# Optimization experiments

Measured on AMD Instinct MI355X. Metric: run time of the kernel, lower is better.

Reference implementation:

```python
import jax, jax.numpy as jnp
import numpy as np

B = 512; S = 6; Q = 2            # meta-batch, n_way*k_shot, n_way*q_query
DIM = 64; IMG = 28; N_WAY = 2
HEADS = 4; HD = DIM // HEADS     # retrieval heads / head dim
EPS = 1e-5


def _pool_mat(inp, out):
    # exact torch AdaptiveAvgPool2d windowing as a matrix [out, inp]
    P = np.zeros((out, inp), np.float32)
    for i in range(out):
        s = (i * inp) // out
        e = -((-(i + 1) * inp) // out)
        P[i, s:e] = 1.0 / (e - s)
    return jnp.asarray(P)

P28 = _pool_mat(IMG, 8)  # 28 -> 8; subsequent 8 -> 8 pools are identity


def _gelu(x):
    return jax.nn.gelu(x, approximate=False)


def _conv(x, w, b):
    y = jax.lax.conv_general_dilated(x, w, (1, 1), ((1, 1), (1, 1)),
                                     dimension_numbers=('NCHW', 'OIHW', 'NCHW'))
    return y + b[None, :, None, None]


def _bn(x, p):
    # p rows: gamma, beta, running_mean, running_var (eval-mode BatchNorm2d)
    g, bt, m, v = p[0], p[1], p[2], p[3]
    sc = g / jnp.sqrt(v + EPS)
    return (x - m[None, :, None, None]) * sc[None, :, None, None] + bt[None, :, None, None]


def _img_in(x, c1w, c1b, bn1, c2w, c2b, bn2, c3w, c3b, bn3, c4w, c4b, bn4, lin_w):
    h = _bn(_conv(x, c1w, c1b), bn1)
    h = jnp.einsum('oi,ncij,pj->ncop', P28, h, P28)   # adaptive avg pool 28x28 -> 8x8
    h = _gelu(h)                                       # dropout is identity in eval
    h = _gelu(_bn(_conv(h, c2w, c2b), bn2))
    h = _gelu(_bn(_conv(h, c3w, c3b), bn3))
    h = _gelu(_bn(_conv(h, c4w, c4b), bn4))            # -> [N,1,8,8]
    h = h.reshape(h.shape[0], -1)                      # [N,64]
    return h @ lin_w.T                                 # Linear(64 -> DIM, no bias)


def _net(x, w1, w2):
    # x: [B,K,D]; w1,w2: [B,D,D] batched fast weights
    h = jnp.einsum('bed,bkd->bke', w1, x)
    ah = _gelu(h)
    y = jnp.einsum('bed,bkd->bke', w2, ah)
    return y, h


def _get_lor(x, w1, w2, r_q, r_k, r_v, r_o, ln_w, ln_b):
    b, k, _ = x.shape
    q, _ = _net(x, w1, w2)
    qh = jnp.einsum('nhd,bkd->bknh', r_q, q)
    sc = jnp.einsum('bknh,rnh->bknr', qh, r_k) / (HD ** 0.5)
    p = jax.nn.softmax(sc, axis=-1)
    lor = jnp.einsum('bknr,rnh->bknh', p, r_v).reshape(b, k, DIM)
    lor = jnp.einsum('de,bkd->bke', r_o, lor)
    z = lor + x
    mu = z.mean(-1, keepdims=True)
    var = ((z - mu) ** 2).mean(-1, keepdims=True)
    return (z - mu) / jnp.sqrt(var + EPS) * ln_w + ln_b


def _forward(query_w, sxs, qxs, inner_lr, c1w, c1b, bn1, c2w, c2b, bn2, c3w, c3b, bn3,
             c4w, c4b, bn4, lin_w, emb, w1, w2, tags, r_q, r_k, r_v, r_o, ln_w, ln_b,
             sys, qys):
    b = query_w.shape[0]
    s = sxs.shape[1]
    q = qxs.shape[1]
    feats = lambda im: _img_in(im.reshape(-1, 1, IMG, IMG), c1w, c1b, bn1, c2w, c2b,
                               bn2, c3w, c3b, bn3, c4w, c4b, bn4, lin_w)
    sx = feats(sxs).reshape(b, s, DIM)
    qx = feats(qxs).reshape(b, q, DIM)
    qe = tags[4]
    w1b = jnp.broadcast_to(w1, (b, DIM, DIM))
    w2b = jnp.broadcast_to(w2, (b, DIM, DIM))
    bound = sx + emb[sys]                                          # [B,S,D]
    # all 4 tag variants for all S shots in one vectorized get_lor call
    inp = (bound[:, :, None, :] + tags[:4][None, None]).reshape(b, s * 4, DIM)
    lors = _get_lor(inp, w1b, w2b, r_q, r_k, r_v, r_o, ln_w, ln_b).reshape(b, s, 4, DIM)
    l1s, r1s, l2s, r2s = lors[:, :, 0], lors[:, :, 1], lors[:, :, 2], lors[:, :, 3]
    qw1 = w1[None] + jnp.einsum('bsl,bsr->blr', l1s, r1s)
    qw2 = w2[None] + jnp.einsum('bsl,bsr->blr', l2s, r2s)
    preds, _ = _net(qx + qe, qw1, qw2)                             # [B,Q,D]
    logits = jnp.einsum('ld,bqd->bql', emb, preds).reshape(-1, N_WAY)
    labels = qys.reshape(-1)
    ls = jax.nn.log_softmax(logits)
    task_loss = -jnp.take_along_axis(ls, labels[:, None], axis=1).mean()
    n_correct = (jnp.argmax(logits, axis=1) == labels).sum()
    return task_loss, n_correct, b * q


def setup_inputs() -> dict:
    key = jax.random.key(0)
    ks = jax.random.split(key, 24)
    rn = lambda i, sh, sc=1.0: sc * jax.random.normal(ks[i], sh, jnp.float32)
    def bnp(i, c):
        k0, k1, k2 = jax.random.split(ks[i], 3)
        return jnp.stack([1.0 + 0.1 * jax.random.normal(k0, (c,)),
                          0.1 * jax.random.normal(k1, (c,)),
                          0.1 * jax.random.normal(k2, (c,)),
                          0.5 + jax.random.uniform(jax.random.fold_in(ks[i], 3), (c,))])
    return {
        'query_w': rn(0, (B, DIM)),
        'sxs': rn(1, (B, S, IMG * IMG)),
        'qxs': rn(2, (B, Q, IMG * IMG)),
        'inner_lr': jnp.float32(0.1),
        'c1w': rn(3, (32, 1, 3, 3), 0.3), 'c1b': rn(4, (32,), 0.1), 'bn1': bnp(5, 32),
        'c2w': rn(6, (32, 32, 3, 3), 0.06), 'c2b': rn(7, (32,), 0.1), 'bn2': bnp(8, 32),
        'c3w': rn(9, (32, 32, 3, 3), 0.06), 'c3b': rn(10, (32,), 0.1), 'bn3': bnp(11, 32),
        'c4w': rn(12, (1, 32, 3, 3), 0.06), 'c4b': rn(13, (1,), 0.1), 'bn4': bnp(14, 1),
        'lin_w': rn(15, (DIM, 64), 0.125),
        'emb': rn(16, (N_WAY, DIM), 0.125),
        'w1': rn(17, (DIM, DIM), 0.125),
        'w2': rn(18, (DIM, DIM), 0.125),
        'tags': rn(19, (8, DIM), 0.125),
        'r_q': rn(20, (HEADS, HD, DIM), 0.125),
        'r_k': rn(21, (16, HEADS, HD), 0.25),
        'r_v': rn(22, (16, HEADS, HD), 0.25),
        'r_o': rn(23, (DIM, DIM), 0.125),
        'ln_w': 0.001 * jnp.ones((DIM,), jnp.float32),
        'ln_b': jnp.zeros((DIM,), jnp.float32),
        'sys': jax.random.randint(jax.random.fold_in(key, 100), (B, S), 0, N_WAY),
        'qys': jax.random.randint(jax.random.fold_in(key, 101), (B, Q), 0, N_WAY),
    }


def reference(query_w, sxs, qxs, inner_lr, c1w, c1b, bn1, c2w, c2b, bn2, c3w, c3b, bn3,
              c4w, c4b, bn4, lin_w, emb, w1, w2, tags, r_q, r_k, r_v, r_o, ln_w, ln_b,
              sys, qys):
    task_loss, n_correct, n_q = _forward(query_w, sxs, qxs, inner_lr, c1w, c1b, bn1,
                                         c2w, c2b, bn2, c3w, c3b, bn3, c4w, c4b, bn4,
                                         lin_w, emb, w1, w2, tags, r_q, r_k, r_v, r_o,
                                         ln_w, ln_b, sys, qys)
    return (task_loss, task_loss, jnp.float32(0.0), n_correct, n_q)
```

## Files before the change

kernel.cpp:

```cpp
#include <hip/hip_runtime.h>
#include <math.h>

constexpr int NSUP = 3072;
constexpr float EPSF = 1e-5f;

constexpr int WS_W1B  = 0;
constexpr int WS_B1   = 1024;
constexpr int WS_W2B  = 1056;
constexpr int WS_W3B  = 5664;
constexpr int WS_W4B  = 10272;
constexpr int WS_B4   = 10416;
constexpr int WS_B2   = 10420;
constexpr int WS_B3   = 10452;
constexpr int WS_HW1  = 10484;
constexpr int WS_HW2  = 12788;
constexpr int WS_HRQ  = 15092;
constexpr int WS_HROT = 17396;
constexpr int WS_PART = 19700;
constexpr int WS_FEATS= 20724;

using short8 = __attribute__((ext_vector_type(8))) short;
using f32x4  = __attribute__((ext_vector_type(4))) float;

__device__ __forceinline__ float gelu_f(float x) {
    return 0.5f * x * (1.0f + erff(x * 0.70710678118654752440f));
}
__device__ __forceinline__ unsigned short f2bf(float f) {
    unsigned u = __float_as_uint(f);
    return (unsigned short)((u + 0x7FFFu + ((u >> 16) & 1u)) >> 16);
}
__device__ __forceinline__ float bflo(unsigned u) { return __uint_as_float(u << 16); }
__device__ __forceinline__ float bfhi(unsigned u) { return __uint_as_float(u & 0xffff0000u); }

__global__ void __launch_bounds__(256) precompute_kernel(
    const float* __restrict__ c1w, const float* __restrict__ c1b, const float* __restrict__ bn1,
    const float* __restrict__ c2w, const float* __restrict__ c2b, const float* __restrict__ bn2,
    const float* __restrict__ c3w, const float* __restrict__ c3b, const float* __restrict__ bn3,
    const float* __restrict__ c4w, const float* __restrict__ c4b, const float* __restrict__ bn4,
    const float* __restrict__ w1, const float* __restrict__ w2,
    const float* __restrict__ rq, const float* __restrict__ ro,
    float* __restrict__ ws)
{
    const int gid = blockIdx.x * 256 + threadIdx.x;
    const int gsz = gridDim.x * 256;

    unsigned short* w1b = (unsigned short*)(ws + WS_W1B);
    for (int v = gid; v < 2048; v += gsz) {
        int kt = v >> 10, rem = v & 1023, oc = rem >> 5, kk = rem & 31;
        int tap = kt * 32 + kk;
        unsigned short o = 0;
        if (tap < 36) {
            int tt = tap / 6, s = tap - tt * 6;
            float sum = 0.f;
            for (int di = 0; di < 3; ++di) {
                int a = tt - di; if (a < 0 || a > 3) continue;
                for (int dj = 0; dj < 3; ++dj) {
                    int bb = s - dj; if (bb < 0 || bb > 3) continue;
                    sum += c1w[oc * 9 + di * 3 + dj];
                }
            }
            float sc1 = bn1[oc] * rsqrtf(bn1[96 + oc] + EPSF);
            o = f2bf(sum * sc1 * (1.0f / 16.0f));
        }
        w1b[v] = o;
    }
    for (int c = gid; c < 32; c += gsz) {
        float sc1 = bn1[c] * rsqrtf(bn1[96 + c] + EPSF);
        ws[WS_B1 + c] = (c1b[c] - bn1[64 + c]) * sc1 + bn1[32 + c];
        float sc2 = bn2[c] * rsqrtf(bn2[96 + c] + EPSF);
        ws[WS_B2 + c] = (c2b[c] - bn2[64 + c]) * sc2 + bn2[32 + c];
        float sc3 = bn3[c] * rsqrtf(bn3[96 + c] + EPSF);
        ws[WS_B3 + c] = (c3b[c] - bn3[64 + c]) * sc3 + bn3[32 + c];
    }
    unsigned short* w2b = (unsigned short*)(ws + WS_W2B);
    unsigned short* w3b = (unsigned short*)(ws + WS_W3B);
    for (int v = gid; v < 9216; v += gsz) {
        int tap = v >> 10, oc = (v >> 5) & 31, ic = v & 31;
        float sc2 = bn2[oc] * rsqrtf(bn2[96 + oc] + EPSF);
        float sc3 = bn3[oc] * rsqrtf(bn3[96 + oc] + EPSF);
        w2b[v] = f2bf(c2w[oc * 288 + ic * 9 + tap] * sc2);
        w3b[v] = f2bf(c3w[oc * 288 + ic * 9 + tap] * sc3);
    }
    {
        unsigned short* w4b = (unsigned short*)(ws + WS_W4B);
        float sc4 = bn4[0] * rsqrtf(bn4[3] + EPSF);
        for (int v = gid; v < 288; v += gsz) {
            int tap = v >> 5, ic = v & 31;
            w4b[v] = f2bf(c4w[ic * 9 + tap] * sc4);
        }
        if (gid == 0) ws[WS_B4] = (c4b[0] - bn4[2]) * sc4 + bn4[1];
    }
    unsigned short* hw1 = (unsigned short*)(ws + WS_HW1);
    unsigned short* hw2 = (unsigned short*)(ws + WS_HW2);
    unsigned short* hrq = (unsigned short*)(ws + WS_HRQ);
    unsigned short* hro = (unsigned short*)(ws + WS_HROT);
    for (int v = gid; v < 4608; v += gsz) {
        int e = v / 72, d = v - e * 72;
        unsigned short a = 0, b = 0, c = 0, r = 0;
        if (d < 64) {
            a = f2bf(w1[e * 64 + d]);
            b = f2bf(w2[e * 64 + d]);
            c = f2bf(rq[e * 64 + d]);
            r = f2bf(ro[d * 64 + e]);
        }
        hw1[v] = a; hw2[v] = b; hrq[v] = c; hro[v] = r;
    }
}

__global__ void __launch_bounds__(512, 4) feats_kernel(
    const float* __restrict__ sxs, const float* __restrict__ qxs,
    const float* __restrict__ lin_w, const float* __restrict__ ws,
    float* __restrict__ feats)
{
    __shared__ __align__(16) unsigned short sAct[8][3200];
    __shared__ __align__(16) unsigned short sWB[9216];
    __shared__ __align__(16) float sh4[8][64];

    const int t    = threadIdx.x;
    const int wv   = t >> 6;
    const int lane = t & 63;
    const int col  = lane & 15;
    const int quad = lane >> 4;
    const int n    = blockIdx.x * 8 + wv;

    unsigned short* A = sAct[wv];

    {
        uint4 z = {0, 0, 0, 0};
        for (int i = t; i < 3200; i += 512) ((uint4*)sAct)[i] = z;
        if (t < 256) ((uint4*)sWB)[t] = ((const uint4*)(ws + WS_W1B))[t];
    }
    __syncthreads();

    {
        const float* img = (n < NSUP) ? (sxs + (size_t)n * 784) : (qxs + (size_t)(n - NSUP) * 784);
        int ttj[8], ssj[8];
        #pragma unroll
        for (int j = 0; j < 8; ++j) {
            int k = quad * 8 + j;
            ttj[j] = k / 6; ssj[j] = k - ttj[j] * 6;
        }
        f32x4 acc[4][2];
        #pragma unroll
        for (int mt = 0; mt < 4; ++mt) { acc[mt][0] = (f32x4){0,0,0,0}; acc[mt][1] = (f32x4){0,0,0,0}; }

        short8 b00 = *(const short8*)(sWB + (0 * 32 + 0 * 16 + col) * 32 + quad * 8);
        short8 b01 = *(const short8*)(sWB + (0 * 32 + 1 * 16 + col) * 32 + quad * 8);
        short8 b10 = *(const short8*)(sWB + (1 * 32 + 0 * 16 + col) * 32 + quad * 8);
        short8 b11 = *(const short8*)(sWB + (1 * 32 + 1 * 16 + col) * 32 + quad * 8);

        #pragma unroll
        for (int mt = 0; mt < 4; ++mt) {
            int px = mt * 16 + col;
            int sr = (((px >> 3) * 7) >> 1) - 1;
            int sc = (((px & 7) * 7) >> 1) - 1;
            short8 a0;
            #pragma unroll
            for (int j = 0; j < 8; ++j) {
                int rr = sr + ttj[j], cc = sc + ssj[j];
                float v = ((unsigned)rr < 28u && (unsigned)cc < 28u) ? img[rr * 28 + cc] : 0.f;
                a0[j] = (short)f2bf(v);
            }
            acc[mt][0] = __builtin_amdgcn_mfma_f32_16x16x32_bf16(a0, b00, acc[mt][0], 0, 0, 0);
            acc[mt][1] = __builtin_amdgcn_mfma_f32_16x16x32_bf16(a0, b01, acc[mt][1], 0, 0, 0);
            short8 a1 = {0,0,0,0,0,0,0,0};
            if (quad == 0) {
                #pragma unroll
                for (int j = 0; j < 4; ++j) {
                    int rr = sr + 5, cc = sc + 2 + j;
                    float v = ((unsigned)rr < 28u && (unsigned)cc < 28u) ? img[rr * 28 + cc] : 0.f;
                    a1[j] = (short)f2bf(v);
                }
            }
            acc[mt][0] = __builtin_amdgcn_mfma_f32_16x16x32_bf16(a1, b10, acc[mt][0], 0, 0, 0);
            acc[mt][1] = __builtin_amdgcn_mfma_f32_16x16x32_bf16(a1, b11, acc[mt][1], 0, 0, 0);
        }
        float bi0 = ws[WS_B1 + col], bi1 = ws[WS_B1 + 16 + col];
        #pragma unroll
        for (int mt = 0; mt < 4; ++mt)
            #pragma unroll
            for (int reg = 0; reg < 4; ++reg) {
                int px = mt * 16 + quad * 4 + reg;
                unsigned short* dst = A + (((px >> 3) + 1) * 10 + (px & 7) + 1) * 32;
                dst[col]      = f2bf(gelu_f(acc[mt][0][reg] + bi0));
                dst[col + 16] = f2bf(gelu_f(acc[mt][1][reg] + bi1));
            }
    }
    __syncthreads();
    for (int i = t; i < 1152; i += 512) ((uint4*)sWB)[i] = ((const uint4*)(ws + WS_W2B))[i];
    __syncthreads();

    #pragma unroll 1
    for (int layer = 0; layer < 2; ++layer) {
        f32x4 acc[4][2];
        #pragma unroll
        for (int mt = 0; mt < 4; ++mt) { acc[mt][0] = (f32x4){0,0,0,0}; acc[mt][1] = (f32x4){0,0,0,0}; }
        const unsigned short* abase[4];
        #pragma unroll
        for (int mt = 0; mt < 4; ++mt) {
            int px = mt * 16 + col;
            abase[mt] = A + ((px >> 3) * 10 + (px & 7)) * 32 + quad * 8;
        }
        #pragma unroll
        for (int dr = 0; dr < 3; ++dr)
            #pragma unroll
            for (int dc = 0; dc < 3; ++dc) {
                int tap = dr * 3 + dc;
                short8 b0 = *(const short8*)(sWB + (tap * 32 + col) * 32 + quad * 8);
                short8 b1 = *(const short8*)(sWB + (tap * 32 + 16 + col) * 32 + quad * 8);
                #pragma unroll
                for (int mt = 0; mt < 4; ++mt) {
                    short8 a = *(const short8*)(abase[mt] + (dr * 10 + dc) * 32);
                    acc[mt][0] = __builtin_amdgcn_mfma_f32_16x16x32_bf16(a, b0, acc[mt][0], 0, 0, 0);
                    acc[mt][1] = __builtin_amdgcn_mfma_f32_16x16x32_bf16(a, b1, acc[mt][1], 0, 0, 0);
                }
            }
        float bi0 = ws[(layer ? WS_B3 : WS_B2) + col];
        float bi1 = ws[(layer ? WS_B3 : WS_B2) + 16 + col];
        #pragma unroll
        for (int mt = 0; mt < 4; ++mt)
            #pragma unroll
            for (int reg = 0; reg < 4; ++reg) {
                int px = mt * 16 + quad * 4 + reg;
                unsigned short* dst = A + (((px >> 3) + 1) * 10 + (px & 7) + 1) * 32;
                dst[col]      = f2bf(gelu_f(acc[mt][0][reg] + bi0));
                dst[col + 16] = f2bf(gelu_f(acc[mt][1][reg] + bi1));
            }
        __syncthreads();
        if (layer == 0) {
            for (int i = t; i < 1152; i += 512) ((uint4*)sWB)[i] = ((const uint4*)(ws + WS_W3B))[i];
            __syncthreads();
        }
    }

    {
        f32x4 acc4[4];
        #pragma unroll
        for (int mt = 0; mt < 4; ++mt) acc4[mt] = (f32x4){0,0,0,0};
        const unsigned short* abase[4];
        #pragma unroll
        for (int mt = 0; mt < 4; ++mt) {
            int px = mt * 16 + col;
            abase[mt] = A + ((px >> 3) * 10 + (px & 7)) * 32 + quad * 8;
        }
        const unsigned short* w4g = (const unsigned short*)(ws + WS_W4B);
        #pragma unroll
        for (int dr = 0; dr < 3; ++dr)
            #pragma unroll
            for (int dc = 0; dc < 3; ++dc) {
                int tap = dr * 3 + dc;
                short8 b = *(const short8*)(w4g + tap * 32 + quad * 8);
                #pragma unroll
                for (int mt = 0; mt < 4; ++mt) {
                    short8 a = *(const short8*)(abase[mt] + (dr * 10 + dc) * 32);
                    acc4[mt] = __builtin_amdgcn_mfma_f32_16x16x32_bf16(a, b, acc4[mt], 0, 0, 0);
                }
            }
        if (col < 4) {
            f32x4 v = acc4[0];
            if (col == 1) v = acc4[1];
            else if (col == 2) v = acc4[2];
            else if (col == 3) v = acc4[3];
            float b4 = ws[WS_B4];
            #pragma unroll
            for (int reg = 0; reg < 4; ++reg)
                sh4[wv][col * 16 + quad * 4 + reg] = gelu_f(v[reg] + b4);
        }
    }
    __syncthreads();

    {
        const float4* lw = (const float4*)(lin_w + (size_t)lane * 64);
        const float4* hp = (const float4*)sh4[wv];
        float acc = 0.f;
        #pragma unroll
        for (int j = 0; j < 16; ++j) {
            float4 w = lw[j], h = hp[j];
            acc += w.x * h.x + w.y * h.y + w.z * h.z + w.w * h.w;
        }
        feats[n * 64 + lane] = acc;
    }
}

__device__ __forceinline__ void head_gemm(const unsigned short* __restrict__ Ab,
                                          const unsigned short* __restrict__ Bw,
                                          int col, int quad, int wvid, f32x4 res[2])
{
    #pragma unroll
    for (int u = 0; u < 2; ++u) {
        int tau = wvid + u * 4;
        int mt = tau & 1, nt = tau >> 1;
        f32x4 acc = {0, 0, 0, 0};
        #pragma unroll
        for (int kt = 0; kt < 2; ++kt) {
            short8 a = *(const short8*)(Ab + (mt * 16 + col) * 72 + kt * 32 + quad * 8);
            short8 b = *(const short8*)(Bw + (nt * 16 + col) * 72 + kt * 32 + quad * 8);
            acc = __builtin_amdgcn_mfma_f32_16x16x32_bf16(a, b, acc, 0, 0, 0);
        }
        res[u] = acc;
    }
}

__global__ void __launch_bounds__(256, 2) head_kernel(
    const float* __restrict__ emb, const float* __restrict__ tags,
    const float* __restrict__ rk, const float* __restrict__ rv,
    const float* __restrict__ lnw, const float* __restrict__ lnb,
    const int* __restrict__ sys, const int* __restrict__ qys,
    const float* __restrict__ ws, const float* __restrict__ feats,
    float* __restrict__ part)
{
    __shared__ __align__(16) unsigned short sW1B[4608], sW2B[4608], sRQB[4608], sROT[4608];
    __shared__ __align__(16) unsigned short bufA[2304], bufB[2304];
    __shared__ __align__(16) float sXf[1536];
    __shared__ __align__(16) float s_xq[128], s_ah[128], s_yp[128];
    __shared__ float s_t1[12], s_t2[12], s_mu[24], s_rs[24], s_lg[4];

    const int t    = threadIdx.x;
    const int b    = blockIdx.x;
    const int wvid = t >> 6;
    const int col  = t & 15;
    const int quad = (t >> 4) & 3;

    for (int i = t; i < 576; i += 256) {
        ((uint4*)sW1B)[i] = ((const uint4*)(ws + WS_HW1))[i];
        ((uint4*)sW2B)[i] = ((const uint4*)(ws + WS_HW2))[i];
        ((uint4*)sRQB)[i] = ((const uint4*)(ws + WS_HRQ))[i];
        ((uint4*)sROT)[i] = ((const uint4*)(ws + WS_HROT))[i];
    }
    if (t < 72) {
        uint4 z = {0, 0, 0, 0};
        ((uint4*)(bufA + 1728))[t] = z;
        ((uint4*)(bufB + 1728))[t] = z;
    }
    for (int idx = t; idx < 1536; idx += 256) {
        int k = idx >> 6, e = idx & 63;
        int s = k >> 2, tg = k & 3;
        int cls = sys[b * 6 + s];
        float v = feats[(b * 6 + s) * 64 + e] + emb[cls * 64 + e] + tags[tg * 64 + e];
        sXf[idx] = v;
        bufA[k * 72 + e] = f2bf(v);
    }
    __syncthreads();

    f32x4 r[2];
    head_gemm(bufA, sW1B, col, quad, wvid, r);
    #pragma unroll
    for (int u = 0; u < 2; ++u) {
        int tau = wvid + u * 4, mt = tau & 1, nt = tau >> 1;
        #pragma unroll
        for (int reg = 0; reg < 4; ++reg) {
            int row = mt * 16 + quad * 4 + reg;
            if (row < 24) bufB[row * 72 + nt * 16 + col] = f2bf(gelu_f(r[u][reg]));
        }
    }
    __syncthreads();
    head_gemm(bufB, sW2B, col, quad, wvid, r);
    #pragma unroll
    for (int u = 0; u < 2; ++u) {
        int tau = wvid + u * 4, mt = tau & 1, nt = tau >> 1;
        #pragma unroll
        for (int reg = 0; reg < 4; ++reg) {
            int row = mt * 16 + quad * 4 + reg;
            if (row < 24) bufA[row * 72 + nt * 16 + col] = f2bf(r[u][reg]);
        }
    }
    __syncthreads();
    head_gemm(bufA, sRQB, col, quad, wvid, r);
    #pragma unroll
    for (int u = 0; u < 2; ++u) {
        int tau = wvid + u * 4, mt = tau & 1, nt = tau >> 1;
        #pragma unroll
        for (int reg = 0; reg < 4; ++reg) {
            int row = mt * 16 + quad * 4 + reg;
            if (row < 24) bufB[row * 72 + nt * 16 + col] = f2bf(r[u][reg]);
        }
    }
    __syncthreads();

    if (t < 96) {
        int k = t >> 2, nn = t & 3;
        const unsigned short* qp = bufB + k * 72 + nn * 16;
        uint4 u0 = *(const uint4*)(qp);
        uint4 u1 = *(const uint4*)(qp + 8);
        float qv[16];
        qv[0]=bflo(u0.x); qv[1]=bfhi(u0.x); qv[2]=bflo(u0.y); qv[3]=bfhi(u0.y);
        qv[4]=bflo(u0.z); qv[5]=bfhi(u0.z); qv[6]=bflo(u0.w); qv[7]=bfhi(u0.w);
        qv[8]=bflo(u1.x); qv[9]=bfhi(u1.x); qv[10]=bflo(u1.y); qv[11]=bfhi(u1.y);
        qv[12]=bflo(u1.z); qv[13]=bfhi(u1.z); qv[14]=bflo(u1.w); qv[15]=bfhi(u1.w);
        float sc[16]; float mx = -1e30f;
        #pragma unroll
        for (int rr = 0; rr < 16; ++rr) {
            const float* kp = rk + rr * 64 + nn * 16;
            float d = 0.f;
            #pragma unroll
            for (int h = 0; h < 16; ++h) d += qv[h] * kp[h];
            d *= 0.25f;
            sc[rr] = d; mx = fmaxf(mx, d);
        }
        float sum = 0.f;
        #pragma unroll
        for (int rr = 0; rr < 16; ++rr) { sc[rr] = expf(sc[rr] - mx); sum += sc[rr]; }
        float inv = 1.0f / sum;
        float o[16];
        #pragma unroll
        for (int h = 0; h < 16; ++h) o[h] = 0.f;
        #pragma unroll
        for (int rr = 0; rr < 16; ++rr) {
            const float* vp = rv + rr * 64 + nn * 16;
            float p = sc[rr];
            #pragma unroll
            for (int h = 0; h < 16; ++h) o[h] += p * vp[h];
        }
        unsigned short* op = bufA + k * 72 + nn * 16;
        #pragma unroll
        for (int h = 0; h < 16; ++h) op[h] = f2bf(o[h] * inv);
    }
    __syncthreads();

    head_gemm(bufA, sROT, col, quad, wvid, r);
    #pragma unroll
    for (int u = 0; u < 2; ++u) {
        int tau = wvid + u * 4, mt = tau & 1, nt = tau >> 1;
        #pragma unroll
        for (int reg = 0; reg < 4; ++reg) {
            int row = mt * 16 + quad * 4 + reg;
            if (row < 24) {
                int idx = row * 64 + nt * 16 + col;
                sXf[idx] = sXf[idx] + r[u][reg];
            }
        }
    }
    __syncthreads();

    if (t < 24) {
        const float4* zp = (const float4*)(sXf + t * 64);
        float sx_ = 0.f;
        #pragma unroll
        for (int j = 0; j < 16; ++j) {
            float4 v = zp[(j + t) & 15];
            sx_ += v.x + v.y + v.z + v.w;
        }
        float mu = sx_ * (1.0f / 64.0f);
        float vv = 0.f;
        #pragma unroll
        for (int j = 0; j < 16; ++j) {
            float4 v = zp[(j + t) & 15];
            float d0 = v.x - mu, d1 = v.y - mu, d2 = v.z - mu, d3 = v.w - mu;
            vv += d0*d0 + d1*d1 + d2*d2 + d3*d3;
        }
        s_mu[t] = mu;
        s_rs[t] = 1.0f / sqrtf(vv * (1.0f / 64.0f) + EPSF);
    }
    __syncthreads();
    for (int idx = t; idx < 1536; idx += 256) {
        int k = idx >> 6, e = idx & 63;
        float v = (sXf[idx] - s_mu[k]) * s_rs[k] * lnw[e] + lnb[e];
        bufB[k * 72 + e] = f2bf(v);
    }
    if (t < 128) {
        int q = t >> 6, e = t & 63;
        s_xq[t] = feats[(NSUP + b * 2 + q) * 64 + e] + tags[256 + e];
    }
    __syncthreads();

    if (t < 12) {
        int q = t / 6, s = t - q * 6;
        const uint4* rp = (const uint4*)(bufB + (s * 4 + 1) * 72);
        const float* xp = s_xq + q * 64;
        float d = 0.f;
        #pragma unroll
        for (int j = 0; j < 8; ++j) {
            uint4 u = rp[j];
            const float* x = xp + j * 8;
            d += bflo(u.x)*x[0] + bfhi(u.x)*x[1] + bflo(u.y)*x[2] + bfhi(u.y)*x[3]
               + bflo(u.z)*x[4] + bfhi(u.z)*x[5] + bflo(u.w)*x[6] + bfhi(u.w)*x[7];
        }
        s_t1[t] = d;
    }
    __syncthreads();
    if (t < 128) {
        int q = t >> 6, e = t & 63;
        const uint4* wp = (const uint4*)(sW1B + e * 72);
        const float* xp = s_xq + q * 64;
        float acc = 0.f;
        #pragma unroll
        for (int j = 0; j < 8; ++j) {
            uint4 u = wp[j];
            const float* x = xp + j * 8;
            acc += bflo(u.x)*x[0] + bfhi(u.x)*x[1] + bflo(u.y)*x[2] + bfhi(u.y)*x[3]
                 + bflo(u.z)*x[4] + bfhi(u.z)*x[5] + bflo(u.w)*x[6] + bfhi(u.w)*x[7];
        }
        #pragma unroll
        for (int s = 0; s < 6; ++s)
            acc += bflo((unsigned)bufB[(s * 4 + 0) * 72 + e]) * s_t1[q * 6 + s];
        s_ah[t] = gelu_f(acc);
    }
    __syncthreads();
    if (t < 12) {
        int q = t / 6, s = t - q * 6;
        const uint4* rp = (const uint4*)(bufB + (s * 4 + 3) * 72);
        const float* xp = s_ah + q * 64;
        float d = 0.f;
        #pragma unroll
        for (int j = 0; j < 8; ++j) {
            uint4 u = rp[j];
            const float* x = xp + j * 8;
            d += bflo(u.x)*x[0] + bfhi(u.x)*x[1] + bflo(u.y)*x[2] + bfhi(u.y)*x[3]
               + bflo(u.z)*x[4] + bfhi(u.z)*x[5] + bflo(u.w)*x[6] + bfhi(u.w)*x[7];
        }
        s_t2[t] = d;
    }
    __syncthreads();
    if (t < 128) {
        int q = t >> 6, e = t & 63;
        const uint4* wp = (const uint4*)(sW2B + e * 72);
        const float* xp = s_ah + q * 64;
        float acc = 0.f;
        #pragma unroll
        for (int j = 0; j < 8; ++j) {
            uint4 u = wp[j];
            const float* x = xp + j * 8;
            acc += bflo(u.x)*x[0] + bfhi(u.x)*x[1] + bflo(u.y)*x[2] + bfhi(u.y)*x[3]
                 + bflo(u.z)*x[4] + bfhi(u.z)*x[5] + bflo(u.w)*x[6] + bfhi(u.w)*x[7];
        }
        #pragma unroll
        for (int s = 0; s < 6; ++s)
            acc += bflo((unsigned)bufB[(s * 4 + 2) * 72 + e]) * s_t2[q * 6 + s];
        s_yp[t] = acc;
    }
    __syncthreads();
    if (t < 4) {
        int q = t >> 1, ll = t & 1;
        const float4* ep = (const float4*)(emb + ll * 64);
        const float4* yp = (const float4*)(s_yp + q * 64);
        float d = 0.f;
        #pragma unroll
        for (int j = 0; j < 16; ++j) {
            float4 a = ep[j], x = yp[j];
            d += a.x*x.x + a.y*x.y + a.z*x.z + a.w*x.w;
        }
        s_lg[t] = d;
    }
    __syncthreads();
    if (t == 0) {
        float lsum = 0.f, corr = 0.f;
        #pragma unroll
        for (int q = 0; q < 2; ++q) {
            float l0 = s_lg[q * 2], l1 = s_lg[q * 2 + 1];
            int lab = qys[b * 2 + q];
            float m = fmaxf(l0, l1);
            float lse = m + logf(expf(l0 - m) + expf(l1 - m));
            lsum += -((lab ? l1 : l0) - lse);
            int pred = (l1 > l0) ? 1 : 0;
            corr += (pred == lab) ? 1.0f : 0.0f;
        }
        part[b] = lsum;
        part[512 + b] = corr;
    }
}

__global__ void __launch_bounds__(256) finalize_kernel(const float* __restrict__ part,
                                                       float* __restrict__ out)
{
    __shared__ float sl[256], sc[256];
    const int t = threadIdx.x;
    sl[t] = part[t] + part[t + 256];
    sc[t] = part[512 + t] + part[768 + t];
    __syncthreads();
    for (int s = 128; s > 0; s >>= 1) {
        if (t < s) { sl[t] += sl[t + s]; sc[t] += sc[t + s]; }
        __syncthreads();
    }
    if (t == 0) {
        float loss = sl[0] * (1.0f / 1024.0f);
        out[0] = loss;
        out[1] = loss;
        out[2] = 0.0f;
        out[3] = sc[0];
        out[4] = 1024.0f;
    }
}

extern "C" void kernel_launch(void* const* d_in, const int* in_sizes, int n_in,
                              void* d_out, int out_size, void* d_ws, size_t ws_size,
                              hipStream_t stream)
{
    (void)in_sizes; (void)n_in; (void)out_size; (void)ws_size;
    const float* sxs  = (const float*)d_in[1];
    const float* qxs  = (const float*)d_in[2];
    const float* c1w  = (const float*)d_in[4];
    const float* c1b  = (const float*)d_in[5];
    const float* bn1  = (const float*)d_in[6];
    const float* c2w  = (const float*)d_in[7];
    const float* c2b  = (const float*)d_in[8];
    const float* bn2  = (const float*)d_in[9];
    const float* c3w  = (const float*)d_in[10];
    const float* c3b  = (const float*)d_in[11];
    const float* bn3  = (const float*)d_in[12];
    const float* c4w  = (const float*)d_in[13];
    const float* c4b  = (const float*)d_in[14];
    const float* bn4  = (const float*)d_in[15];
    const float* lin_w= (const float*)d_in[16];
    const float* emb  = (const float*)d_in[17];
    const float* w1   = (const float*)d_in[18];
    const float* w2   = (const float*)d_in[19];
    const float* tags = (const float*)d_in[20];
    const float* rq   = (const float*)d_in[21];
    const float* rk   = (const float*)d_in[22];
    const float* rv   = (const float*)d_in[23];
    const float* ro   = (const float*)d_in[24];
    const float* lnw  = (const float*)d_in[25];
    const float* lnb  = (const float*)d_in[26];
    const int*   sys  = (const int*)d_in[27];
    const int*   qys  = (const int*)d_in[28];

    float* ws  = (float*)d_ws;
    float* out = (float*)d_out;

    precompute_kernel<<<64, 256, 0, stream>>>(c1w, c1b, bn1, c2w, c2b, bn2,
                                              c3w, c3b, bn3, c4w, c4b, bn4,
                                              w1, w2, rq, ro, ws);
    feats_kernel<<<512, 512, 0, stream>>>(sxs, qxs, lin_w, ws, ws + WS_FEATS);
    head_kernel<<<512, 256, 0, stream>>>(emb, tags, rk, rv, lnw, lnb, sys, qys,
                                         ws, ws + WS_FEATS, ws + WS_PART);
    finalize_kernel<<<1, 256, 0, stream>>>(ws + WS_PART, out);
}
```

Measured before the change: 182.7 us.

## Stage image in LDS, prefetch conv weights, fast GELU and softmax exp

The feats kernel now loads each image once into LDS as bf16 with coalesced float4 reads, and the im2col gather reads from LDS instead of doing scattered global loads. Only the padding border is zeroed, not the whole buffer. The conv2 and conv3 weights are prefetched into registers so their global latency overlaps earlier compute, conv4 weights are staged in LDS, and one barrier is dropped. GELU swaps erff for an Abramowitz–Stegun polynomial with a fast exp and reciprocal, and the head kernel stages rk/rv in LDS and uses __expf. The approximations trade some accuracy for speed, and the extra register and LDS use may reduce occupancy.

```diff
diff --git a/kernel.cpp b/kernel.cpp
--- a/kernel.cpp
+++ b/kernel.cpp
@@ -23,7 +23,19 @@
 using f32x4  = __attribute__((ext_vector_type(4))) float;
 
 __device__ __forceinline__ float gelu_f(float x) {
-    return 0.5f * x * (1.0f + erff(x * 0.70710678118654752440f));
+    float z  = fabsf(x) * 0.70710678118654752440f;
+    float t  = __builtin_amdgcn_rcpf(__builtin_fmaf(0.3275911f, z, 1.0f));
+    float p  = t * __builtin_fmaf(t,
+                 __builtin_fmaf(t,
+                   __builtin_fmaf(t,
+                     __builtin_fmaf(t, 1.061405429f, -1.453152027f),
+                     1.421413741f),
+                   -0.284496736f),
+                 0.254829592f);
+    float e  = __expf(-z * z);
+    float er = __builtin_fmaf(-p, e, 1.0f);
+    float s  = copysignf(er, x);
+    return 0.5f * x * (1.0f + s);
 }
 __device__ __forceinline__ unsigned short f2bf(float f) {
     unsigned u = __float_as_uint(f);
@@ -107,6 +119,44 @@
     }
 }
 
+__device__ __forceinline__ void conv32(unsigned short* __restrict__ A,
+                                       const unsigned short* __restrict__ W,
+                                       float bi0, float bi1, int col, int quad)
+{
+    f32x4 acc[4][2];
+    #pragma unroll
+    for (int mt = 0; mt < 4; ++mt) { acc[mt][0] = (f32x4){0,0,0,0}; acc[mt][1] = (f32x4){0,0,0,0}; }
+    const unsigned short* abase[4];
+    #pragma unroll
+    for (int mt = 0; mt < 4; ++mt) {
+        int px = mt * 16 + col;
+        abase[mt] = A + ((px >> 3) * 10 + (px & 7)) * 32 + quad * 8;
+    }
+    #pragma unroll
+    for (int dr = 0; dr < 3; ++dr)
+        #pragma unroll
+        for (int dc = 0; dc < 3; ++dc) {
+            int tap = dr * 3 + dc;
+            short8 b0 = *(const short8*)(W + (tap * 32 + col) * 32 + quad * 8);
+            short8 b1 = *(const short8*)(W + (tap * 32 + 16 + col) * 32 + quad * 8);
+            #pragma unroll
+            for (int mt = 0; mt < 4; ++mt) {
+                short8 a = *(const short8*)(abase[mt] + (dr * 10 + dc) * 32);
+                acc[mt][0] = __builtin_amdgcn_mfma_f32_16x16x32_bf16(a, b0, acc[mt][0], 0, 0, 0);
+                acc[mt][1] = __builtin_amdgcn_mfma_f32_16x16x32_bf16(a, b1, acc[mt][1], 0, 0, 0);
+            }
+        }
+    #pragma unroll
+    for (int mt = 0; mt < 4; ++mt)
+        #pragma unroll
+        for (int reg = 0; reg < 4; ++reg) {
+            int px = mt * 16 + quad * 4 + reg;
+            unsigned short* dst = A + (((px >> 3) + 1) * 10 + (px & 7) + 1) * 32;
+            dst[col]      = f2bf(gelu_f(acc[mt][0][reg] + bi0));
+            dst[col + 16] = f2bf(gelu_f(acc[mt][1][reg] + bi1));
+        }
+}
+
 __global__ void __launch_bounds__(512, 4) feats_kernel(
     const float* __restrict__ sxs, const float* __restrict__ qxs,
     const float* __restrict__ lin_w, const float* __restrict__ ws,
@@ -114,6 +164,7 @@
 {
     __shared__ __align__(16) unsigned short sAct[8][3200];
     __shared__ __align__(16) unsigned short sWB[9216];
+    __shared__ __align__(16) unsigned short sW4[288];
     __shared__ __align__(16) float sh4[8][64];
 
     const int t    = threadIdx.x;
@@ -125,15 +176,29 @@
 
     unsigned short* A = sAct[wv];
 
-    {
-        uint4 z = {0, 0, 0, 0};
-        for (int i = t; i < 3200; i += 512) ((uint4*)sAct)[i] = z;
-        if (t < 256) ((uint4*)sWB)[t] = ((const uint4*)(ws + WS_W1B))[t];
-    }
-    __syncthreads();
+    const uint4* w2v = (const uint4*)(ws + WS_W2B);
+    uint4 pw0 = w2v[t];
+    uint4 pw1 = w2v[t + 512];
+    uint4 pw2 = {0, 0, 0, 0};
+    if (t < 128) pw2 = w2v[t + 1024];
 
     {
         const float* img = (n < NSUP) ? (sxs + (size_t)n * 784) : (qxs + (size_t)(n - NSUP) * 784);
+        const float4* sv = (const float4*)img;
+        #pragma unroll
+        for (int j = 0; j < 4; ++j) {
+            int idx = j * 64 + lane;
+            if (idx < 196) {
+                float4 v = sv[idx];
+                ushort4 o = { f2bf(v.x), f2bf(v.y), f2bf(v.z), f2bf(v.w) };
+                *(ushort4*)(A + idx * 4) = o;
+            }
+        }
+    }
+    if (t < 256) ((uint4*)sWB)[t] = ((const uint4*)(ws + WS_W1B))[t];
+    __syncthreads();
+
+    {
         int ttj[8], ssj[8];
         #pragma unroll
         for (int j = 0; j < 8; ++j) {
@@ -158,8 +223,10 @@
             #pragma unroll
             for (int j = 0; j < 8; ++j) {
                 int rr = sr + ttj[j], cc = sc + ssj[j];
-                float v = ((unsigned)rr < 28u && (unsigned)cc < 28u) ? img[rr * 28 + cc] : 0.f;
-                a0[j] = (short)f2bf(v);
+                bool ok = ((unsigned)rr < 28u) && ((unsigned)cc < 28u);
+                int off = ok ? (rr * 28 + cc) : 0;
+                unsigned short hv = A[off];
+                a0[j] = ok ? (short)hv : (short)0;
             }
             acc[mt][0] = __builtin_amdgcn_mfma_f32_16x16x32_bf16(a0, b00, acc[mt][0], 0, 0, 0);
             acc[mt][1] = __builtin_amdgcn_mfma_f32_16x16x32_bf16(a0, b01, acc[mt][1], 0, 0, 0);
@@ -168,12 +235,32 @@
                 #pragma unroll
                 for (int j = 0; j < 4; ++j) {
                     int rr = sr + 5, cc = sc + 2 + j;
-                    float v = ((unsigned)rr < 28u && (unsigned)cc < 28u) ? img[rr * 28 + cc] : 0.f;
-                    a1[j] = (short)f2bf(v);
+                    bool ok = ((unsigned)rr < 28u) && ((unsigned)cc < 28u);
+                    int off = ok ? (rr * 28 + cc) : 0;
+                    unsigned short hv = A[off];
+                    a1[j] = ok ? (short)hv : (short)0;
                 }
             }
             acc[mt][0] = __builtin_amdgcn_mfma_f32_16x16x32_bf16(a1, b10, acc[mt][0], 0, 0, 0);
             acc[mt][1] = __builtin_amdgcn_mfma_f32_16x16x32_bf16(a1, b11, acc[mt][1], 0, 0, 0);
+        }
+
+        {
+            uint4 z4 = {0, 0, 0, 0};
+            #pragma unroll
+            for (int it = 0; it < 3; ++it) {
+                int h = lane + it * 64;
+                if (h < 144) {
+                    int u4;
+                    if (h < 40)      u4 = h;
+                    else if (h < 80) u4 = 360 + (h - 40);
+                    else {
+                        int k = h - 80; int r = 1 + (k >> 3); int cj = k & 7;
+                        u4 = r * 40 + ((cj >= 4) ? (32 + cj) : cj);
+                    }
+                    ((uint4*)A)[u4] = z4;
+                }
+            }
         }
         float bi0 = ws[WS_B1 + col], bi1 = ws[WS_B1 + 16 + col];
         #pragma unroll
@@ -187,14 +274,33 @@
             }
     }
     __syncthreads();
-    for (int i = t; i < 1152; i += 512) ((uint4*)sWB)[i] = ((const uint4*)(ws + WS_W2B))[i];
-    __syncthreads();
-
-    #pragma unroll 1
-    for (int layer = 0; layer < 2; ++layer) {
-        f32x4 acc[4][2];
-        #pragma unroll
-        for (int mt = 0; mt < 4; ++mt) { acc[mt][0] = (f32x4){0,0,0,0}; acc[mt][1] = (f32x4){0,0,0,0}; }
+
+    {
+        ((uint4*)sWB)[t]       = pw0;
+        ((uint4*)sWB)[t + 512] = pw1;
+        if (t < 128) ((uint4*)sWB)[t + 1024] = pw2;
+        if (t < 36)  ((uint4*)sW4)[t] = ((const uint4*)(ws + WS_W4B))[t];
+        const uint4* w3v = (const uint4*)(ws + WS_W3B);
+        pw0 = w3v[t];
+        pw1 = w3v[t + 512];
+        if (t < 128) pw2 = w3v[t + 1024];
+    }
+    __syncthreads();
+
+    conv32(A, sWB, ws[WS_B2 + col], ws[WS_B2 + 16 + col], col, quad);
+    __syncthreads();
+    {
+        ((uint4*)sWB)[t]       = pw0;
+        ((uint4*)sWB)[t + 512] = pw1;
+        if (t < 128) ((uint4*)sWB)[t + 1024] = pw2;
+    }
+    __syncthreads();
+    conv32(A, sWB, ws[WS_B3 + col], ws[WS_B3 + 16 + col], col, quad);
+
+    {
+        f32x4 acc4[4];
+        #pragma unroll
+        for (int mt = 0; mt < 4; ++mt) acc4[mt] = (f32x4){0,0,0,0};
         const unsigned short* abase[4];
         #pragma unroll
         for (int mt = 0; mt < 4; ++mt) {
@@ -206,50 +312,7 @@
             #pragma unroll
             for (int dc = 0; dc < 3; ++dc) {
                 int tap = dr * 3 + dc;
-                short8 b0 = *(const short8*)(sWB + (tap * 32 + col) * 32 + quad * 8);
-                short8 b1 = *(const short8*)(sWB + (tap * 32 + 16 + col) * 32 + quad * 8);
-                #pragma unroll
-                for (int mt = 0; mt < 4; ++mt) {
-                    short8 a = *(const short8*)(abase[mt] + (dr * 10 + dc) * 32);
-                    acc[mt][0] = __builtin_amdgcn_mfma_f32_16x16x32_bf16(a, b0, acc[mt][0], 0, 0, 0);
-                    acc[mt][1] = __builtin_amdgcn_mfma_f32_16x16x32_bf16(a, b1, acc[mt][1], 0, 0, 0);
-                }
-            }
-        float bi0 = ws[(layer ? WS_B3 : WS_B2) + col];
-        float bi1 = ws[(layer ? WS_B3 : WS_B2) + 16 + col];
-        #pragma unroll
-        for (int mt = 0; mt < 4; ++mt)
-            #pragma unroll
-            for (int reg = 0; reg < 4; ++reg) {
-                int px = mt * 16 + quad * 4 + reg;
-                unsigned short* dst = A + (((px >> 3) + 1) * 10 + (px & 7) + 1) * 32;
-                dst[col]      = f2bf(gelu_f(acc[mt][0][reg] + bi0));
-                dst[col + 16] = f2bf(gelu_f(acc[mt][1][reg] + bi1));
-            }
-        __syncthreads();
-        if (layer == 0) {
-            for (int i = t; i < 1152; i += 512) ((uint4*)sWB)[i] = ((const uint4*)(ws + WS_W3B))[i];
-            __syncthreads();
-        }
-    }
-
-    {
-        f32x4 acc4[4];
-        #pragma unroll
-        for (int mt = 0; mt < 4; ++mt) acc4[mt] = (f32x4){0,0,0,0};
-        const unsigned short* abase[4];
-        #pragma unroll
-        for (int mt = 0; mt < 4; ++mt) {
-            int px = mt * 16 + col;
-            abase[mt] = A + ((px >> 3) * 10 + (px & 7)) * 32 + quad * 8;
-        }
-        const unsigned short* w4g = (const unsigned short*)(ws + WS_W4B);
-        #pragma unroll
-        for (int dr = 0; dr < 3; ++dr)
-            #pragma unroll
-            for (int dc = 0; dc < 3; ++dc) {
-                int tap = dr * 3 + dc;
-                short8 b = *(const short8*)(w4g + tap * 32 + quad * 8);
+                short8 b = *(const short8*)(sW4 + tap * 32 + quad * 8);
                 #pragma unroll
                 for (int mt = 0; mt < 4; ++mt) {
                     short8 a = *(const short8*)(abase[mt] + (dr * 10 + dc) * 32);
@@ -267,7 +330,6 @@
                 sh4[wv][col * 16 + quad * 4 + reg] = gelu_f(v[reg] + b4);
         }
     }
-    __syncthreads();
 
     {
         const float4* lw = (const float4*)(lin_w + (size_t)lane * 64);
@@ -312,6 +374,7 @@
     __shared__ __align__(16) unsigned short sW1B[4608], sW2B[4608], sRQB[4608], sROT[4608];
     __shared__ __align__(16) unsigned short bufA[2304], bufB[2304];
     __shared__ __align__(16) float sXf[1536];
+    __shared__ __align__(16) float sRK[1024], sRV[1024];
     __shared__ __align__(16) float s_xq[128], s_ah[128], s_yp[128];
     __shared__ float s_t1[12], s_t2[12], s_mu[24], s_rs[24], s_lg[4];
 
@@ -321,6 +384,8 @@
     const int col  = t & 15;
     const int quad = (t >> 4) & 3;
 
+    ((float4*)sRK)[t] = ((const float4*)rk)[t];
+    ((float4*)sRV)[t] = ((const float4*)rv)[t];
     for (int i = t; i < 576; i += 256) {
         ((uint4*)sW1B)[i] = ((const uint4*)(ws + WS_HW1))[i];
         ((uint4*)sW2B)[i] = ((const uint4*)(ws + WS_HW2))[i];
@@ -390,7 +455,7 @@
         float sc[16]; float mx = -1e30f;
         #pragma unroll
         for (int rr = 0; rr < 16; ++rr) {
-            const float* kp = rk + rr * 64 + nn * 16;
+            const float* kp = sRK + rr * 64 + nn * 16;
             float d = 0.f;
             #pragma unroll
             for (int h = 0; h < 16; ++h) d += qv[h] * kp[h];
@@ -399,14 +464,14 @@
         }
         float sum = 0.f;
         #pragma unroll
-        for (int rr = 0; rr < 16; ++rr) { sc[rr] = expf(sc[rr] - mx); sum += sc[rr]; }
+        for (int rr = 0; rr < 16; ++rr) { sc[rr] = __expf(sc[rr] - mx); sum += sc[rr]; }
         float inv = 1.0f / sum;
         float o[16];
         #pragma unroll
         for (int h = 0; h < 16; ++h) o[h] = 0.f;
         #pragma unroll
         for (int rr = 0; rr < 16; ++rr) {
-            const float* vp = rv + rr * 64 + nn * 16;
+            const float* vp = sRV + rr * 64 + nn * 16;
             float p = sc[rr];
             #pragma unroll
             for (int h = 0; h < 16; ++h) o[h] += p * vp[h];
```

Measured after the change: 168.7 us. 1.08x faster.
